# Optimization experiments

Measured on AMD Instinct MI355X. Metric: run time of the kernel, lower is better.

Reference implementation:

```python
import jax, jax.numpy as jnp
import numpy as np

D_MODEL = 512
N_HEADS = 8
D_K = D_MODEL // N_HEADS


def setup_inputs() -> dict:
    key = jax.random.key(0)
    ks = jax.random.split(key, 7)
    s = 1.0 / np.sqrt(D_MODEL)
    return {
        "x": jax.random.normal(ks[0], (2, 4096, D_MODEL), dtype=jnp.float32),
        "W_q": jax.random.normal(ks[1], (D_MODEL, D_MODEL), dtype=jnp.float32) * s,
        "W_k": jax.random.normal(ks[2], (D_MODEL, D_MODEL), dtype=jnp.float32) * s,
        "W_v": jax.random.normal(ks[3], (D_MODEL, D_MODEL), dtype=jnp.float32) * s,
        "b_v": jax.random.normal(ks[4], (D_MODEL,), dtype=jnp.float32) * s,
        "W_o": jax.random.normal(ks[5], (D_MODEL, D_MODEL), dtype=jnp.float32) * s,
        "b_o": jax.random.normal(ks[6], (D_MODEL,), dtype=jnp.float32) * s,
    }


def _split_heads(t):
    # [N, S, d_model] -> [N, H, S, d_k]
    N, S, _ = t.shape
    return t.reshape(N, S, N_HEADS, D_K).transpose(0, 2, 1, 3)


def reference(x, W_q, W_k, W_v, b_v, W_o, b_o):
    N, S, _ = x.shape
    # nn.Linear computes x @ W.T (+ b)
    Q = _split_heads(x @ W_q.T)
    K = _split_heads(x @ W_k.T)
    V = _split_heads(x @ W_v.T + b_v)
    scale = jnp.sqrt(jnp.asarray(D_K, x.dtype))
    scores = jnp.einsum('nhqd,nhkd->nhqk', Q, K) / scale  # [N,H,S,S]
    causal = jnp.tril(jnp.ones((S, S), dtype=bool))
    scores = jnp.where(causal, scores, -jnp.inf)
    attn = jax.nn.softmax(scores, axis=-1)
    out = jnp.einsum('nhqk,nhkd->nhqd', attn, V)  # [N,H,S,d_k]
    out = out.transpose(0, 2, 1, 3).reshape(N, S, D_MODEL)
    return out @ W_o.T + b_o
```

## Files before the change

### kernel.cpp

```cpp
#include <hip/hip_runtime.h>
#include <hip/hip_bf16.h>

#define NB 2
#define SEQ 4096
#define DM 512
#define NH 8
#define DKH 64
#define MTOT (NB*SEQ)

typedef __attribute__((ext_vector_type(4))) float f32x4;
typedef __attribute__((ext_vector_type(16))) float f32x16;
typedef __attribute__((ext_vector_type(8))) short bf16x8;
typedef __attribute__((ext_vector_type(2))) unsigned uint2v;

__device__ inline unsigned short f2bf(float f) {
    union { float f; unsigned int u; } v; v.f = f;
    unsigned int r = v.u + 0x7FFFu + ((v.u >> 16) & 1u);
    return (unsigned short)(r >> 16);
}

#define QSCALE 0.18033688011112042f

__global__ void cast_kernel(const float* __restrict__ x, const float* __restrict__ wq,
                            const float* __restrict__ wk, const float* __restrict__ wv,
                            const float* __restrict__ wo, unsigned short* __restrict__ dst) {
    const int NX = MTOT*DM;
    const int NW = DM*DM;
    int i4 = blockIdx.x * blockDim.x + threadIdx.x;
    long e = (long)i4 * 4;
    if (e >= NX + 4L*NW) return;
    const float* src; long off;
    if (e < NX)           { src = x;  off = e; }
    else if (e < NX+NW)   { src = wq; off = e - NX; }
    else if (e < NX+2*NW) { src = wk; off = e - NX - NW; }
    else if (e < NX+3*NW) { src = wv; off = e - NX - 2*NW; }
    else                  { src = wo; off = e - NX - 3*NW; }
    float4 v = *reinterpret_cast<const float4*>(src + off);
    ushort4 o;
    o.x = f2bf(v.x); o.y = f2bf(v.y); o.z = f2bf(v.z); o.w = f2bf(v.w);
    *reinterpret_cast<ushort4*>(dst + e) = o;
}

#define GEMM_KLOOP(APTR, BPTR, BROW, BCOL)                                         \
    f32x4 acc[4][4] = {};                                                          \
    for (int kt = 0; kt < 8; ++kt) {                                               \
        __syncthreads();                                                           \
        _Pragma("unroll")                                                          \
        for (int i = 0; i < 4; ++i) {                                              \
            int rbase = i*32 + wid*8;                                              \
            int row = rbase + (lane >> 3);                                         \
            int csrc = (lane & 7) ^ (row & 7);                                     \
            const unsigned short* asrc = Aptr_ + (long)((BROW)+row)*512 + kt*64 + csrc*8; \
            __builtin_amdgcn_global_load_lds(                                      \
                (const __attribute__((address_space(1))) unsigned int*)asrc,       \
                (__attribute__((address_space(3))) unsigned int*)&As[rbase*64], 16, 0, 0); \
            const unsigned short* bsrc = Bptr_ + (long)((BCOL)+row)*512 + kt*64 + csrc*8; \
            __builtin_amdgcn_global_load_lds(                                      \
                (const __attribute__((address_space(1))) unsigned int*)bsrc,       \
                (__attribute__((address_space(3))) unsigned int*)&Bs[rbase*64], 16, 0, 0); \
        }                                                                          \
        __syncthreads();                                                           \
        _Pragma("unroll")                                                          \
        for (int kk = 0; kk < 2; ++kk) {                                           \
            bf16x8 af[4], bfr[4];                                                  \
            _Pragma("unroll")                                                      \
            for (int mi = 0; mi < 4; ++mi) {                                       \
                int row = wr*64 + mi*16 + l15;                                     \
                int colb = (kk*32 + l4*8) * 2;                                     \
                af[mi] = *reinterpret_cast<const bf16x8*>(                         \
                    reinterpret_cast<const char*>(As) + row*128 + (colb ^ ((row&7)<<4))); \
            }                                                                      \
            _Pragma("unroll")                                                      \
            for (int ni = 0; ni < 4; ++ni) {                                       \
                int row = wc*64 + ni*16 + l15;                                     \
                int colb = (kk*32 + l4*8) * 2;                                     \
                bfr[ni] = *reinterpret_cast<const bf16x8*>(                        \
                    reinterpret_cast<const char*>(Bs) + row*128 + (colb ^ ((row&7)<<4))); \
            }                                                                      \
            _Pragma("unroll")                                                      \
            for (int mi = 0; mi < 4; ++mi)                                         \
                _Pragma("unroll")                                                  \
                for (int ni = 0; ni < 4; ++ni)                                     \
                    acc[mi][ni] = __builtin_amdgcn_mfma_f32_16x16x32_bf16(af[mi], bfr[ni], acc[mi][ni], 0, 0, 0); \
        }                                                                          \
    }

__global__ __launch_bounds__(256, 2) void gemm_qk(
    const unsigned short* __restrict__ A,
    const unsigned short* __restrict__ B,
    unsigned short* __restrict__ Qh, unsigned short* __restrict__ Kh)
{
    __shared__ __align__(16) unsigned short As[128*64];
    __shared__ __align__(16) unsigned short Bs[128*64];
    int tid = threadIdx.x;
    int wid = tid >> 6, lane = tid & 63;
    int wr = wid >> 1, wc = wid & 1;
    int brow = blockIdx.x * 128;
    int bcol = blockIdx.y * 128;
    int l15 = lane & 15, l4 = lane >> 4;
    const unsigned short* Aptr_ = A;
    const unsigned short* Bptr_ = B;

    GEMM_KLOOP(A, B, brow, bcol)

    #pragma unroll
    for (int mi = 0; mi < 4; ++mi) {
        #pragma unroll
        for (int ni = 0; ni < 4; ++ni) {
            #pragma unroll
            for (int r = 0; r < 4; ++r) {
                int row = brow + wr*64 + mi*16 + l4*4 + r;
                int col = bcol + wc*64 + ni*16 + l15;
                float v = acc[mi][ni][r];
                int which = col >> 9;
                int cw = col & 511;
                int h = cw >> 6, d = cw & 63;
                int b = row >> 12, s = row & 4095;
                int bh = b*NH + h;
                if (which == 0)
                    Qh[((long)(bh*SEQ + s))*DKH + d] = f2bf(v * QSCALE);
                else
                    Kh[((long)(bh*SEQ + s))*DKH + d] = f2bf(v);
            }
        }
    }
}

__global__ __launch_bounds__(256, 2) void gemm_v(
    const unsigned short* __restrict__ A,
    const unsigned short* __restrict__ B,
    const float* __restrict__ bv,
    unsigned short* __restrict__ Vt)
{
    __shared__ __align__(16) unsigned short As[128*64];
    __shared__ __align__(16) unsigned short Bs[128*64];
    __shared__ __align__(16) unsigned short Trs[128*136];
    int tid = threadIdx.x;
    int wid = tid >> 6, lane = tid & 63;
    int wr = wid >> 1, wc = wid & 1;
    int brow = blockIdx.x * 128;
    int bcol = 1024 + blockIdx.y * 128;
    int l15 = lane & 15, l4 = lane >> 4;
    const unsigned short* Aptr_ = A;
    const unsigned short* Bptr_ = B;

    GEMM_KLOOP(A, B, brow, bcol)

    #pragma unroll
    for (int mi = 0; mi < 4; ++mi) {
        #pragma unroll
        for (int ni = 0; ni < 4; ++ni) {
            #pragma unroll
            for (int r = 0; r < 4; ++r) {
                int rowLoc = wr*64 + mi*16 + l4*4 + r;
                int colLoc = wc*64 + ni*16 + l15;
                Trs[colLoc*136 + rowLoc] = f2bf(acc[mi][ni][r] + bv[(bcol + colLoc) & 511]);
            }
        }
    }
    __syncthreads();

    const int b = brow >> 12;
    const int stile = brow & 4095;
    const int hbase = (bcol - 1024) >> 6;
    #pragma unroll
    for (int pass = 0; pass < 8; ++pass) {
        int idx = pass*256 + tid;
        int dd = idx >> 4;
        int s8 = (idx & 15) << 3;
        bf16x8 vv = *reinterpret_cast<const bf16x8*>(&Trs[dd*136 + s8]);
        int bh = b*NH + hbase + (dd >> 6);
        int d = dd & 63;
        *reinterpret_cast<bf16x8*>(Vt + ((long)(bh*DKH + d))*SEQ + stile + s8) = vv;
    }
}

__global__ __launch_bounds__(256, 2) void gemm_out(
    const unsigned short* __restrict__ A,
    const unsigned short* __restrict__ B,
    const float* __restrict__ bias, float* __restrict__ Cout)
{
    __shared__ __align__(16) unsigned short As[128*64];
    __shared__ __align__(16) unsigned short Bs[128*64];
    int tid = threadIdx.x;
    int wid = tid >> 6, lane = tid & 63;
    int wr = wid >> 1, wc = wid & 1;
    int brow = blockIdx.x * 128;
    int bcol = blockIdx.y * 128;
    int l15 = lane & 15, l4 = lane >> 4;
    const unsigned short* Aptr_ = A;
    const unsigned short* Bptr_ = B;

    GEMM_KLOOP(A, B, brow, bcol)

    #pragma unroll
    for (int mi = 0; mi < 4; ++mi) {
        #pragma unroll
        for (int ni = 0; ni < 4; ++ni) {
            #pragma unroll
            for (int r = 0; r < 4; ++r) {
                int row = brow + wr*64 + mi*16 + l4*4 + r;
                int col = bcol + wc*64 + ni*16 + l15;
                Cout[(long)row*DM + col] = acc[mi][ni][r] + bias[col];
            }
        }
    }
}

#define PV_STEP_M(SV, VLS, KS, B0, OD0, OD1, LS)  do {                             \
        unsigned c0, c1, c2, c3;                                                   \
        float t0 = SV[B0+0], t1 = SV[B0+1], t2 = SV[B0+2], t3 = SV[B0+3];          \
        float t4 = SV[B0+4], t5 = SV[B0+5], t6 = SV[B0+6], t7 = SV[B0+7];          \
        asm("v_cvt_pk_bf16_f32 %0, %1, %2" : "=v"(c0) : "v"(t0), "v"(t1));         \
        asm("v_cvt_pk_bf16_f32 %0, %1, %2" : "=v"(c1) : "v"(t2), "v"(t3));         \
        asm("v_cvt_pk_bf16_f32 %0, %1, %2" : "=v"(c2) : "v"(t4), "v"(t5));         \
        asm("v_cvt_pk_bf16_f32 %0, %1, %2" : "=v"(c3) : "v"(t6), "v"(t7));         \
        uint2v sw0 = __builtin_amdgcn_permlane32_swap(c0, c2, false, false);       \
        uint2v sw1 = __builtin_amdgcn_permlane32_swap(c1, c3, false, false);       \
        union { unsigned u[4]; bf16x8 v; } pu;                                     \
        pu.u[0] = sw0[0]; pu.u[1] = sw1[0]; pu.u[2] = sw0[1]; pu.u[3] = sw1[1];    \
        bf16x8 vf0 = *reinterpret_cast<const bf16x8*>(VLS + l31*128      + (((KS)*32 + hi*16) ^ swz)); \
        OD0 = __builtin_amdgcn_mfma_f32_32x32x16_bf16(vf0, pu.v, OD0, 0, 0, 0);    \
        bf16x8 vf1 = *reinterpret_cast<const bf16x8*>(VLS + (32+l31)*128 + (((KS)*32 + hi*16) ^ swz)); \
        OD1 = __builtin_amdgcn_mfma_f32_32x32x16_bf16(vf1, pu.v, OD1, 0, 0, 0);    \
        LS  = __builtin_amdgcn_mfma_f32_32x32x16_bf16(onesv, pu.v, LS, 0, 0, 0);   \
    } while (0)

__global__ __launch_bounds__(256, 2) void attn_fm(
    const unsigned short* __restrict__ Qh,
    const unsigned short* __restrict__ Kh,
    const unsigned short* __restrict__ Vt,
    unsigned short* __restrict__ Obf)
{
    __shared__ __align__(16) unsigned short Klds[2][2][64*64];
    __shared__ __align__(16) unsigned short Vlds[2][2][64*64];
    const int tid = threadIdx.x;
    const int wid = tid >> 6, lane = tid & 63;
    const int g = wid & 1, p = wid >> 1;
    const int l31 = lane & 31;
    const int hi  = lane >> 5;
    const int bh  = blockIdx.x;
    const int j   = blockIdx.y;

    const unsigned short* Qbase = Qh + (long)bh*SEQ*DKH;
    const unsigned short* Kbase = Kh + (long)bh*SEQ*DKH;
    const unsigned short* Vbase = Vt + (long)bh*DKH*SEQ;
    const int swz = (l31 & 7) << 4;

    bf16x8 onesv;
    #pragma unroll
    for (int e = 0; e < 8; ++e) onesv[e] = (short)0x3F80;

    auto STAGE1 = [&](int pb, int b, int key0) {
        #pragma unroll
        for (int ii = 0; ii < 2; ++ii) {
            const int rbase = wid*16 + ii*8;
            const int row = rbase + (lane >> 3);
            const int ck = (lane & 7) ^ (row & 7);
            const unsigned short* ksrc = Kbase + (long)(key0 + row)*DKH + ck*8;
            __builtin_amdgcn_global_load_lds(
                (const __attribute__((address_space(1))) unsigned int*)ksrc,
                (__attribute__((address_space(3))) unsigned int*)&Klds[pb][b][rbase*64], 16, 0, 0);
            const unsigned short* vsrc = Vbase + (long)row*SEQ + key0 + ck*8;
            __builtin_amdgcn_global_load_lds(
                (const __attribute__((address_space(1))) unsigned int*)vsrc,
                (__attribute__((address_space(3))) unsigned int*)&Vlds[pb][b][rbase*64], 16, 0, 0);
        }
    };

    #pragma unroll 1
    for (int half = 0; half < 2; ++half) {
        const int tile = half ? (int)j : 63 - (int)j;
        const int q0w = tile*64 + g*32;
        const int q   = q0w + l31;
        const int nss = (tile >> 1) + 1;

        bf16x8 qf[4];
        #pragma unroll
        for (int kk = 0; kk < 4; ++kk)
            qf[kk] = *reinterpret_cast<const bf16x8*>(Qbase + (long)q*DKH + kk*16 + hi*8);

        f32x16 od0 = {}, od1 = {}, ls = {};

        STAGE1(0, 0, 0);
        if (tile >= 1) STAGE1(1, 0, 64);
        __syncthreads();

        #pragma unroll 1
        for (int ss = 0; ss < nss; ++ss) {
            const int nb = (ss + 1) & 1;
            if (2*(ss+1)     <= tile) STAGE1(0, nb, (2*(ss+1))     << 6);
            if (2*(ss+1) + 1 <= tile) STAGE1(1, nb, (2*(ss+1) + 1) << 6);

            const int kb = 2*ss + p;
            if (kb <= tile) {
                const int key0 = kb << 6;
                const char* kl = reinterpret_cast<const char*>(&Klds[p][ss & 1][0]);
                const char* vl = reinterpret_cast<const char*>(&Vlds[p][ss & 1][0]);

                bf16x8 kfr[4][2];
                #pragma unroll
                for (int kk = 0; kk < 4; ++kk) {
                    const int co = (kk*32 + hi*16) ^ swz;
                    kfr[kk][0] = *reinterpret_cast<const bf16x8*>(kl + l31*128      + co);
                    kfr[kk][1] = *reinterpret_cast<const bf16x8*>(kl + (32+l31)*128 + co);
                }
                f32x16 s0 = {}, s1 = {};
                __builtin_amdgcn_s_setprio(1);
                #pragma unroll
                for (int kk = 0; kk < 4; ++kk) {
                    s0 = __builtin_amdgcn_mfma_f32_32x32x16_bf16(kfr[kk][0], qf[kk], s0, 0, 0, 0);
                    s1 = __builtin_amdgcn_mfma_f32_32x32x16_bf16(kfr[kk][1], qf[kk], s1, 0, 0, 0);
                }
                __builtin_amdgcn_s_setprio(0);

                if (kb == tile) {
                    #pragma unroll
                    for (int r = 0; r < 16; ++r) {
                        const int ko = (r&3) + 8*(r>>2) + 4*hi;
                        if (key0 + ko > q)      s0[r] = -1e30f;
                        if (key0 + 32 + ko > q) s1[r] = -1e30f;
                    }
                }

                #pragma unroll
                for (int r = 0; r < 16; ++r) {
                    s0[r] = __builtin_amdgcn_exp2f(s0[r]);
                    s1[r] = __builtin_amdgcn_exp2f(s1[r]);
                }

                __builtin_amdgcn_s_setprio(1);
                PV_STEP_M(s0, vl, 0, 0, od0, od1, ls);
                PV_STEP_M(s0, vl, 1, 8, od0, od1, ls);
                PV_STEP_M(s1, vl, 2, 0, od0, od1, ls);
                PV_STEP_M(s1, vl, 3, 8, od0, od1, ls);
                __builtin_amdgcn_s_setprio(0);
            }
            __syncthreads();
        }

        float lsum = ls[0];
        char*  sod = reinterpret_cast<char*>(&Klds[g][0][0]);
        float* sml = reinterpret_cast<float*>(&Klds[g][1][0]);
        const int lswz = (lane & 7) << 4;
        if (p == 1) {
            #pragma unroll
            for (int i = 0; i < 4; ++i) {
                *reinterpret_cast<f32x4*>(sod + lane*128 + ((i*16) ^ lswz)) =
                    (f32x4){od0[i*4+0], od0[i*4+1], od0[i*4+2], od0[i*4+3]};
                *reinterpret_cast<f32x4*>(sod + lane*128 + (((i+4)*16) ^ lswz)) =
                    (f32x4){od1[i*4+0], od1[i*4+1], od1[i*4+2], od1[i*4+3]};
            }
            sml[lane] = lsum;
        }
        __syncthreads();
        if (p == 0) {
            lsum += sml[lane];
            #pragma unroll
            for (int i = 0; i < 4; ++i) {
                f32x4 t0 = *reinterpret_cast<const f32x4*>(sod + lane*128 + ((i*16) ^ lswz));
                f32x4 t1 = *reinterpret_cast<const f32x4*>(sod + lane*128 + (((i+4)*16) ^ lswz));
                #pragma unroll
                for (int k = 0; k < 4; ++k) {
                    od0[i*4+k] += t0[k];
                    od1[i*4+k] += t1[k];
                }
            }
            const float rls = 1.0f / lsum;
            const long obase = (long)((bh >> 3)*SEQ + q)*DM + (bh & 7)*DKH;
            #pragma unroll
            for (int rr = 0; rr < 4; ++rr) {
                ushort4 w0, w1;
                w0.x = f2bf(od0[rr*4+0]*rls); w0.y = f2bf(od0[rr*4+1]*rls);
                w0.z = f2bf(od0[rr*4+2]*rls); w0.w = f2bf(od0[rr*4+3]*rls);
                *reinterpret_cast<ushort4*>(Obf + obase + rr*8 + hi*4) = w0;
                w1.x = f2bf(od1[rr*4+0]*rls); w1.y = f2bf(od1[rr*4+1]*rls);
                w1.z = f2bf(od1[rr*4+2]*rls); w1.w = f2bf(od1[rr*4+3]*rls);
                *reinterpret_cast<ushort4*>(Obf + obase + 32 + rr*8 + hi*4) = w1;
            }
        }
        __syncthreads();
    }
}

extern "C" void kernel_launch(void* const* d_in, const int* in_sizes, int n_in,
                              void* d_out, int out_size, void* d_ws, size_t ws_size,
                              hipStream_t stream) {
    const float* x  = (const float*)d_in[0];
    const float* wq = (const float*)d_in[1];
    const float* wk = (const float*)d_in[2];
    const float* wv = (const float*)d_in[3];
    const float* bv = (const float*)d_in[4];
    const float* wo = (const float*)d_in[5];
    const float* bo = (const float*)d_in[6];
    float* out = (float*)d_out;

    unsigned short* ws = (unsigned short*)d_ws;
    unsigned short* Xbf  = ws;
    unsigned short* Wqkv = Xbf  + 4194304;
    unsigned short* Wob  = Wqkv + 786432;
    unsigned short* Qh   = Wob  + 262144;
    unsigned short* Kh   = Qh   + 4194304;
    unsigned short* Vt   = Kh   + 4194304;
    unsigned short* Obf  = Vt   + 4194304;

    cast_kernel<<<5120, 256, 0, stream>>>(x, wq, wk, wv, wo, Xbf);

    dim3 gqk(64, 8);
    gemm_qk<<<gqk, 256, 0, stream>>>(Xbf, Wqkv, Qh, Kh);
    dim3 gv(64, 4);
    gemm_v<<<gv, 256, 0, stream>>>(Xbf, Wqkv, bv, Vt);

    dim3 ga(16, 32);
    attn_fm<<<ga, 256, 0, stream>>>(Qh, Kh, Vt, Obf);

    dim3 go(64, 4);
    gemm_out<<<go, 256, 0, stream>>>(Obf, Wob, bo, out);
}
```

Baseline: 100.4 us.

## Split key halves across waves so each wave covers all 64 queries

Reassigns attention work so each wave processes both 32-query halves of the tile against its own 32-key half of a key block. K and V fragment LDS reads per wave drop, and the K fragments are reused across two query groups. The cost is more live accumulators and Q fragments, which raises register pressure. The final combine also becomes a 4-way LDS reduction done by a single wave.

```diff
diff --git a/kernel.cpp b/kernel.cpp
--- a/kernel.cpp
+++ b/kernel.cpp
@@ -207,7 +207,7 @@
     }
 }
 
-#define PV_STEP_M(SV, VLS, KS, B0, OD0, OD1, LS)  do {                             \
+#define REPACK(SV, B0, PU) do {                                                    \
         unsigned c0, c1, c2, c3;                                                   \
         float t0 = SV[B0+0], t1 = SV[B0+1], t2 = SV[B0+2], t3 = SV[B0+3];          \
         float t4 = SV[B0+4], t5 = SV[B0+5], t6 = SV[B0+6], t7 = SV[B0+7];          \
@@ -217,13 +217,21 @@
         asm("v_cvt_pk_bf16_f32 %0, %1, %2" : "=v"(c3) : "v"(t6), "v"(t7));         \
         uint2v sw0 = __builtin_amdgcn_permlane32_swap(c0, c2, false, false);       \
         uint2v sw1 = __builtin_amdgcn_permlane32_swap(c1, c3, false, false);       \
-        union { unsigned u[4]; bf16x8 v; } pu;                                     \
-        pu.u[0] = sw0[0]; pu.u[1] = sw1[0]; pu.u[2] = sw0[1]; pu.u[3] = sw1[1];    \
+        PU.u[0] = sw0[0]; PU.u[1] = sw1[0]; PU.u[2] = sw0[1]; PU.u[3] = sw1[1];    \
+    } while (0)
+
+#define PV2(SA, SB, VLS, KS, B0) do {                                              \
+        union { unsigned u[4]; bf16x8 v; } puA, puB;                               \
+        REPACK(SA, B0, puA);                                                       \
+        REPACK(SB, B0, puB);                                                       \
         bf16x8 vf0 = *reinterpret_cast<const bf16x8*>(VLS + l31*128      + (((KS)*32 + hi*16) ^ swz)); \
-        OD0 = __builtin_amdgcn_mfma_f32_32x32x16_bf16(vf0, pu.v, OD0, 0, 0, 0);    \
         bf16x8 vf1 = *reinterpret_cast<const bf16x8*>(VLS + (32+l31)*128 + (((KS)*32 + hi*16) ^ swz)); \
-        OD1 = __builtin_amdgcn_mfma_f32_32x32x16_bf16(vf1, pu.v, OD1, 0, 0, 0);    \
-        LS  = __builtin_amdgcn_mfma_f32_32x32x16_bf16(onesv, pu.v, LS, 0, 0, 0);   \
+        odA0 = __builtin_amdgcn_mfma_f32_32x32x16_bf16(vf0, puA.v, odA0, 0, 0, 0); \
+        odA1 = __builtin_amdgcn_mfma_f32_32x32x16_bf16(vf1, puA.v, odA1, 0, 0, 0); \
+        odB0 = __builtin_amdgcn_mfma_f32_32x32x16_bf16(vf0, puB.v, odB0, 0, 0, 0); \
+        odB1 = __builtin_amdgcn_mfma_f32_32x32x16_bf16(vf1, puB.v, odB1, 0, 0, 0); \
+        lsA  = __builtin_amdgcn_mfma_f32_32x32x16_bf16(onesv, puA.v, lsA, 0, 0, 0);\
+        lsB  = __builtin_amdgcn_mfma_f32_32x32x16_bf16(onesv, puB.v, lsB, 0, 0, 0);\
     } while (0)
 
 __global__ __launch_bounds__(256, 2) void attn_fm(
@@ -236,7 +244,7 @@
     __shared__ __align__(16) unsigned short Vlds[2][2][64*64];
     const int tid = threadIdx.x;
     const int wid = tid >> 6, lane = tid & 63;
-    const int g = wid & 1, p = wid >> 1;
+    const int p = wid & 1, h = wid >> 1;
     const int l31 = lane & 31;
     const int hi  = lane >> 5;
     const int bh  = blockIdx.x;
@@ -267,20 +275,27 @@
                 (__attribute__((address_space(3))) unsigned int*)&Vlds[pb][b][rbase*64], 16, 0, 0);
         }
     };
+    auto blk = [&](int b) -> char* {
+        return (b < 4) ? (reinterpret_cast<char*>(&Klds[0][0][0]) + b*8192)
+                       : (reinterpret_cast<char*>(&Vlds[0][0][0]) + (b-4)*8192);
+    };
+    float* smlBase = reinterpret_cast<float*>(reinterpret_cast<char*>(&Vlds[0][0][0]) + 16384);
 
     #pragma unroll 1
     for (int half = 0; half < 2; ++half) {
         const int tile = half ? (int)j : 63 - (int)j;
-        const int q0w = tile*64 + g*32;
-        const int q   = q0w + l31;
+        const int qA = tile*64 + l31;
+        const int qB = qA + 32;
         const int nss = (tile >> 1) + 1;
 
-        bf16x8 qf[4];
+        bf16x8 qfA[4], qfB[4];
         #pragma unroll
-        for (int kk = 0; kk < 4; ++kk)
-            qf[kk] = *reinterpret_cast<const bf16x8*>(Qbase + (long)q*DKH + kk*16 + hi*8);
-
-        f32x16 od0 = {}, od1 = {}, ls = {};
+        for (int kk = 0; kk < 4; ++kk) {
+            qfA[kk] = *reinterpret_cast<const bf16x8*>(Qbase + (long)qA*DKH + kk*16 + hi*8);
+            qfB[kk] = *reinterpret_cast<const bf16x8*>(Qbase + (long)qB*DKH + kk*16 + hi*8);
+        }
+
+        f32x16 odA0 = {}, odA1 = {}, odB0 = {}, odB1 = {}, lsA = {}, lsB = {};
 
         STAGE1(0, 0, 0);
         if (tile >= 1) STAGE1(1, 0, 64);
@@ -294,89 +309,107 @@
 
             const int kb = 2*ss + p;
             if (kb <= tile) {
-                const int key0 = kb << 6;
-                const char* kl = reinterpret_cast<const char*>(&Klds[p][ss & 1][0]);
+                const char* kl = reinterpret_cast<const char*>(&Klds[p][ss & 1][0]) + h*32*128;
                 const char* vl = reinterpret_cast<const char*>(&Vlds[p][ss & 1][0]);
-
-                bf16x8 kfr[4][2];
+                const int key0h = (kb << 6) + (h << 5);
+
+                bf16x8 kfr[4];
                 #pragma unroll
-                for (int kk = 0; kk < 4; ++kk) {
-                    const int co = (kk*32 + hi*16) ^ swz;
-                    kfr[kk][0] = *reinterpret_cast<const bf16x8*>(kl + l31*128      + co);
-                    kfr[kk][1] = *reinterpret_cast<const bf16x8*>(kl + (32+l31)*128 + co);
-                }
-                f32x16 s0 = {}, s1 = {};
+                for (int kk = 0; kk < 4; ++kk)
+                    kfr[kk] = *reinterpret_cast<const bf16x8*>(kl + l31*128 + ((kk*32 + hi*16) ^ swz));
+                f32x16 sA = {}, sB = {};
                 __builtin_amdgcn_s_setprio(1);
                 #pragma unroll
                 for (int kk = 0; kk < 4; ++kk) {
-                    s0 = __builtin_amdgcn_mfma_f32_32x32x16_bf16(kfr[kk][0], qf[kk], s0, 0, 0, 0);
-                    s1 = __builtin_amdgcn_mfma_f32_32x32x16_bf16(kfr[kk][1], qf[kk], s1, 0, 0, 0);
+                    sA = __builtin_amdgcn_mfma_f32_32x32x16_bf16(kfr[kk], qfA[kk], sA, 0, 0, 0);
+                    sB = __builtin_amdgcn_mfma_f32_32x32x16_bf16(kfr[kk], qfB[kk], sB, 0, 0, 0);
                 }
                 __builtin_amdgcn_s_setprio(0);
 
                 if (kb == tile) {
                     #pragma unroll
                     for (int r = 0; r < 16; ++r) {
-                        const int ko = (r&3) + 8*(r>>2) + 4*hi;
-                        if (key0 + ko > q)      s0[r] = -1e30f;
-                        if (key0 + 32 + ko > q) s1[r] = -1e30f;
+                        const int ko = key0h + (r&3) + 8*(r>>2) + 4*hi;
+                        if (ko > qA) sA[r] = -1e30f;
+                        if (ko > qB) sB[r] = -1e30f;
                     }
                 }
 
                 #pragma unroll
                 for (int r = 0; r < 16; ++r) {
-                    s0[r] = __builtin_amdgcn_exp2f(s0[r]);
-                    s1[r] = __builtin_amdgcn_exp2f(s1[r]);
+                    sA[r] = __builtin_amdgcn_exp2f(sA[r]);
+                    sB[r] = __builtin_amdgcn_exp2f(sB[r]);
                 }
 
                 __builtin_amdgcn_s_setprio(1);
-                PV_STEP_M(s0, vl, 0, 0, od0, od1, ls);
-                PV_STEP_M(s0, vl, 1, 8, od0, od1, ls);
-                PV_STEP_M(s1, vl, 2, 0, od0, od1, ls);
-                PV_STEP_M(s1, vl, 3, 8, od0, od1, ls);
+                PV2(sA, sB, vl, (2*h),     0);
+                PV2(sA, sB, vl, (2*h + 1), 8);
                 __builtin_amdgcn_s_setprio(0);
             }
             __syncthreads();
         }
 
-        float lsum = ls[0];
-        char*  sod = reinterpret_cast<char*>(&Klds[g][0][0]);
-        float* sml = reinterpret_cast<float*>(&Klds[g][1][0]);
+        float lA = lsA[0], lB = lsB[0];
         const int lswz = (lane & 7) << 4;
-        if (p == 1) {
+        if (wid != 0) {
+            char* dA = blk((wid-1)*2);
+            char* dB = blk((wid-1)*2 + 1);
             #pragma unroll
             for (int i = 0; i < 4; ++i) {
-                *reinterpret_cast<f32x4*>(sod + lane*128 + ((i*16) ^ lswz)) =
-                    (f32x4){od0[i*4+0], od0[i*4+1], od0[i*4+2], od0[i*4+3]};
-                *reinterpret_cast<f32x4*>(sod + lane*128 + (((i+4)*16) ^ lswz)) =
-                    (f32x4){od1[i*4+0], od1[i*4+1], od1[i*4+2], od1[i*4+3]};
-            }
-            sml[lane] = lsum;
+                *reinterpret_cast<f32x4*>(dA + lane*128 + ((i*16) ^ lswz)) =
+                    (f32x4){odA0[i*4+0], odA0[i*4+1], odA0[i*4+2], odA0[i*4+3]};
+                *reinterpret_cast<f32x4*>(dA + lane*128 + (((i+4)*16) ^ lswz)) =
+                    (f32x4){odA1[i*4+0], odA1[i*4+1], odA1[i*4+2], odA1[i*4+3]};
+                *reinterpret_cast<f32x4*>(dB + lane*128 + ((i*16) ^ lswz)) =
+                    (f32x4){odB0[i*4+0], odB0[i*4+1], odB0[i*4+2], odB0[i*4+3]};
+                *reinterpret_cast<f32x4*>(dB + lane*128 + (((i+4)*16) ^ lswz)) =
+                    (f32x4){odB1[i*4+0], odB1[i*4+1], odB1[i*4+2], odB1[i*4+3]};
+            }
+            smlBase[(wid-1)*128 + lane*2]     = lA;
+            smlBase[(wid-1)*128 + lane*2 + 1] = lB;
         }
         __syncthreads();
-        if (p == 0) {
-            lsum += sml[lane];
-            #pragma unroll
-            for (int i = 0; i < 4; ++i) {
-                f32x4 t0 = *reinterpret_cast<const f32x4*>(sod + lane*128 + ((i*16) ^ lswz));
-                f32x4 t1 = *reinterpret_cast<const f32x4*>(sod + lane*128 + (((i+4)*16) ^ lswz));
+        if (wid == 0) {
+            #pragma unroll 1
+            for (int w = 1; w <= 3; ++w) {
+                const char* dA = blk((w-1)*2);
+                const char* dB = blk((w-1)*2 + 1);
+                lA += smlBase[(w-1)*128 + lane*2];
+                lB += smlBase[(w-1)*128 + lane*2 + 1];
                 #pragma unroll
-                for (int k = 0; k < 4; ++k) {
-                    od0[i*4+k] += t0[k];
-                    od1[i*4+k] += t1[k];
+                for (int i = 0; i < 4; ++i) {
+                    f32x4 tA0 = *reinterpret_cast<const f32x4*>(dA + lane*128 + ((i*16) ^ lswz));
+                    f32x4 tA1 = *reinterpret_cast<const f32x4*>(dA + lane*128 + (((i+4)*16) ^ lswz));
+                    f32x4 tB0 = *reinterpret_cast<const f32x4*>(dB + lane*128 + ((i*16) ^ lswz));
+                    f32x4 tB1 = *reinterpret_cast<const f32x4*>(dB + lane*128 + (((i+4)*16) ^ lswz));
+                    #pragma unroll
+                    for (int k = 0; k < 4; ++k) {
+                        odA0[i*4+k] += tA0[k];
+                        odA1[i*4+k] += tA1[k];
+                        odB0[i*4+k] += tB0[k];
+                        odB1[i*4+k] += tB1[k];
+                    }
                 }
             }
-            const float rls = 1.0f / lsum;
-            const long obase = (long)((bh >> 3)*SEQ + q)*DM + (bh & 7)*DKH;
+            const float rlsA = 1.0f / lA;
+            const float rlsB = 1.0f / lB;
+            const long obaseA = (long)((bh >> 3)*SEQ + qA)*DM + (bh & 7)*DKH;
+            const long obaseB = (long)((bh >> 3)*SEQ + qB)*DM + (bh & 7)*DKH;
             #pragma unroll
             for (int rr = 0; rr < 4; ++rr) {
                 ushort4 w0, w1;
-                w0.x = f2bf(od0[rr*4+0]*rls); w0.y = f2bf(od0[rr*4+1]*rls);
-                w0.z = f2bf(od0[rr*4+2]*rls); w0.w = f2bf(od0[rr*4+3]*rls);
-                *reinterpret_cast<ushort4*>(Obf + obase + rr*8 + hi*4) = w0;
-                w1.x = f2bf(od1[rr*4+0]*rls); w1.y = f2bf(od1[rr*4+1]*rls);
-                w1.z = f2bf(od1[rr*4+2]*rls); w1.w = f2bf(od1[rr*4+3]*rls);
-                *reinterpret_cast<ushort4*>(Obf + obase + 32 + rr*8 + hi*4) = w1;
+                w0.x = f2bf(odA0[rr*4+0]*rlsA); w0.y = f2bf(odA0[rr*4+1]*rlsA);
+                w0.z = f2bf(odA0[rr*4+2]*rlsA); w0.w = f2bf(odA0[rr*4+3]*rlsA);
+                *reinterpret_cast<ushort4*>(Obf + obaseA + rr*8 + hi*4) = w0;
+                w1.x = f2bf(odA1[rr*4+0]*rlsA); w1.y = f2bf(odA1[rr*4+1]*rlsA);
+                w1.z = f2bf(odA1[rr*4+2]*rlsA); w1.w = f2bf(odA1[rr*4+3]*rlsA);
+                *reinterpret_cast<ushort4*>(Obf + obaseA + 32 + rr*8 + hi*4) = w1;
+                w0.x = f2bf(odB0[rr*4+0]*rlsB); w0.y = f2bf(odB0[rr*4+1]*rlsB);
+                w0.z = f2bf(odB0[rr*4+2]*rlsB); w0.w = f2bf(odB0[rr*4+3]*rlsB);
+                *reinterpret_cast<ushort4*>(Obf + obaseB + rr*8 + hi*4) = w0;
+                w1.x = f2bf(odB1[rr*4+0]*rlsB); w1.y = f2bf(odB1[rr*4+1]*rlsB);
+                w1.z = f2bf(odB1[rr*4+2]*rlsB); w1.w = f2bf(odB1[rr*4+3]*rlsB);
+                *reinterpret_cast<ushort4*>(Obf + obaseB + 32 + rr*8 + hi*4) = w1;
             }
         }
         __syncthreads();
```

Result: slower. 102.9 us (+2.5%).

## Restructure attention to one query tile per block with XCD-aware ordering

Applied to the files above, without the earlier changes.

Replaces the paired-tile load balancing (each block handled tiles 63-j and j) with one 64-query tile per block over a 1D grid of 1024 blocks. Blocks are ordered largest tile first and mapped so each head stays on one XCD. The two wave pairs now split each 64-key block into two 32-key halves rather than alternating whole key blocks. LDS is halved to allow 4 blocks per CU. This targets better occupancy and L2 locality, but it depends on the scheduler to balance uneven causal work, and the 32-key split gives each wave less work per barrier.

```diff
diff --git a/kernel.cpp b/kernel.cpp
--- a/kernel.cpp
+++ b/kernel.cpp
@@ -226,32 +226,45 @@
         LS  = __builtin_amdgcn_mfma_f32_32x32x16_bf16(onesv, pu.v, LS, 0, 0, 0);   \
     } while (0)
 
-__global__ __launch_bounds__(256, 2) void attn_fm(
+__global__ __launch_bounds__(256, 4) void attn_fm(
     const unsigned short* __restrict__ Qh,
     const unsigned short* __restrict__ Kh,
     const unsigned short* __restrict__ Vt,
     unsigned short* __restrict__ Obf)
 {
-    __shared__ __align__(16) unsigned short Klds[2][2][64*64];
-    __shared__ __align__(16) unsigned short Vlds[2][2][64*64];
+    __shared__ __align__(16) unsigned short Kc[2][64*64];
+    __shared__ __align__(16) unsigned short Vc[2][64*64];
     const int tid = threadIdx.x;
     const int wid = tid >> 6, lane = tid & 63;
     const int g = wid & 1, p = wid >> 1;
     const int l31 = lane & 31;
     const int hi  = lane >> 5;
-    const int bh  = blockIdx.x;
-    const int j   = blockIdx.y;
+
+    const int id   = blockIdx.x;
+    const int xcd  = id & 7;
+    const int rest = id >> 3;
+    const int bh   = xcd + ((rest & 1) << 3);
+    const int t    = 63 - (rest >> 1);
 
     const unsigned short* Qbase = Qh + (long)bh*SEQ*DKH;
     const unsigned short* Kbase = Kh + (long)bh*SEQ*DKH;
     const unsigned short* Vbase = Vt + (long)bh*DKH*SEQ;
+
+    const int q0w = t*64 + g*32;
+    const int q   = q0w + l31;
+    const int nu  = t + 1;
     const int swz = (l31 & 7) << 4;
 
+    bf16x8 qf[4];
+    #pragma unroll
+    for (int kk = 0; kk < 4; ++kk)
+        qf[kk] = *reinterpret_cast<const bf16x8*>(Qbase + (long)q*DKH + kk*16 + hi*8);
+
     bf16x8 onesv;
     #pragma unroll
     for (int e = 0; e < 8; ++e) onesv[e] = (short)0x3F80;
 
-    auto STAGE1 = [&](int pb, int b, int key0) {
+    auto STAGE = [&](int b, int key0) {
         #pragma unroll
         for (int ii = 0; ii < 2; ++ii) {
             const int rbase = wid*16 + ii*8;
@@ -260,126 +273,98 @@
             const unsigned short* ksrc = Kbase + (long)(key0 + row)*DKH + ck*8;
             __builtin_amdgcn_global_load_lds(
                 (const __attribute__((address_space(1))) unsigned int*)ksrc,
-                (__attribute__((address_space(3))) unsigned int*)&Klds[pb][b][rbase*64], 16, 0, 0);
+                (__attribute__((address_space(3))) unsigned int*)&Kc[b][rbase*64], 16, 0, 0);
             const unsigned short* vsrc = Vbase + (long)row*SEQ + key0 + ck*8;
             __builtin_amdgcn_global_load_lds(
                 (const __attribute__((address_space(1))) unsigned int*)vsrc,
-                (__attribute__((address_space(3))) unsigned int*)&Vlds[pb][b][rbase*64], 16, 0, 0);
+                (__attribute__((address_space(3))) unsigned int*)&Vc[b][rbase*64], 16, 0, 0);
         }
     };
 
+    f32x16 od0 = {}, od1 = {}, ls = {};
+
+    STAGE(0, 0);
+    __syncthreads();
+    int cur = 0;
+
     #pragma unroll 1
-    for (int half = 0; half < 2; ++half) {
-        const int tile = half ? (int)j : 63 - (int)j;
-        const int q0w = tile*64 + g*32;
-        const int q   = q0w + l31;
-        const int nss = (tile >> 1) + 1;
-
-        bf16x8 qf[4];
+    for (int u = 0; u < nu; ++u) {
+        if (u + 1 < nu) STAGE(cur ^ 1, (u + 1) << 6);
+        const char* kl = reinterpret_cast<const char*>(&Kc[cur][0]) + p*32*128;
+        const char* vl = reinterpret_cast<const char*>(&Vc[cur][0]);
+
+        bf16x8 kfr[4];
         #pragma unroll
         for (int kk = 0; kk < 4; ++kk)
-            qf[kk] = *reinterpret_cast<const bf16x8*>(Qbase + (long)q*DKH + kk*16 + hi*8);
-
-        f32x16 od0 = {}, od1 = {}, ls = {};
-
-        STAGE1(0, 0, 0);
-        if (tile >= 1) STAGE1(1, 0, 64);
+            kfr[kk] = *reinterpret_cast<const bf16x8*>(kl + l31*128 + ((kk*32 + hi*16) ^ swz));
+        f32x16 sv = {};
+        __builtin_amdgcn_s_setprio(1);
+        #pragma unroll
+        for (int kk = 0; kk < 4; ++kk)
+            sv = __builtin_amdgcn_mfma_f32_32x32x16_bf16(kfr[kk], qf[kk], sv, 0, 0, 0);
+        __builtin_amdgcn_s_setprio(0);
+
+        if (u == t) {
+            const int kbase = (u << 6) + (p << 5);
+            #pragma unroll
+            for (int r = 0; r < 16; ++r) {
+                const int ko = (r&3) + 8*(r>>2) + 4*hi;
+                if (kbase + ko > q) sv[r] = -1e30f;
+            }
+        }
+
+        #pragma unroll
+        for (int r = 0; r < 16; ++r)
+            sv[r] = __builtin_amdgcn_exp2f(sv[r]);
+
+        __builtin_amdgcn_s_setprio(1);
+        PV_STEP_M(sv, vl, (2*p),     0, od0, od1, ls);
+        PV_STEP_M(sv, vl, (2*p + 1), 8, od0, od1, ls);
+        __builtin_amdgcn_s_setprio(0);
+
         __syncthreads();
-
-        #pragma unroll 1
-        for (int ss = 0; ss < nss; ++ss) {
-            const int nb = (ss + 1) & 1;
-            if (2*(ss+1)     <= tile) STAGE1(0, nb, (2*(ss+1))     << 6);
-            if (2*(ss+1) + 1 <= tile) STAGE1(1, nb, (2*(ss+1) + 1) << 6);
-
-            const int kb = 2*ss + p;
-            if (kb <= tile) {
-                const int key0 = kb << 6;
-                const char* kl = reinterpret_cast<const char*>(&Klds[p][ss & 1][0]);
-                const char* vl = reinterpret_cast<const char*>(&Vlds[p][ss & 1][0]);
-
-                bf16x8 kfr[4][2];
-                #pragma unroll
-                for (int kk = 0; kk < 4; ++kk) {
-                    const int co = (kk*32 + hi*16) ^ swz;
-                    kfr[kk][0] = *reinterpret_cast<const bf16x8*>(kl + l31*128      + co);
-                    kfr[kk][1] = *reinterpret_cast<const bf16x8*>(kl + (32+l31)*128 + co);
-                }
-                f32x16 s0 = {}, s1 = {};
-                __builtin_amdgcn_s_setprio(1);
-                #pragma unroll
-                for (int kk = 0; kk < 4; ++kk) {
-                    s0 = __builtin_amdgcn_mfma_f32_32x32x16_bf16(kfr[kk][0], qf[kk], s0, 0, 0, 0);
-                    s1 = __builtin_amdgcn_mfma_f32_32x32x16_bf16(kfr[kk][1], qf[kk], s1, 0, 0, 0);
-                }
-                __builtin_amdgcn_s_setprio(0);
-
-                if (kb == tile) {
-                    #pragma unroll
-                    for (int r = 0; r < 16; ++r) {
-                        const int ko = (r&3) + 8*(r>>2) + 4*hi;
-                        if (key0 + ko > q)      s0[r] = -1e30f;
-                        if (key0 + 32 + ko > q) s1[r] = -1e30f;
-                    }
-                }
-
-                #pragma unroll
-                for (int r = 0; r < 16; ++r) {
-                    s0[r] = __builtin_amdgcn_exp2f(s0[r]);
-                    s1[r] = __builtin_amdgcn_exp2f(s1[r]);
-                }
-
-                __builtin_amdgcn_s_setprio(1);
-                PV_STEP_M(s0, vl, 0, 0, od0, od1, ls);
-                PV_STEP_M(s0, vl, 1, 8, od0, od1, ls);
-                PV_STEP_M(s1, vl, 2, 0, od0, od1, ls);
-                PV_STEP_M(s1, vl, 3, 8, od0, od1, ls);
-                __builtin_amdgcn_s_setprio(0);
+        cur ^= 1;
+    }
+
+    float lsum = ls[0];
+    char*  sod = reinterpret_cast<char*>(&Kc[g][0]);
+    float* sml = reinterpret_cast<float*>(&Vc[g][0]);
+    const int lswz = (lane & 7) << 4;
+    if (p == 1) {
+        #pragma unroll
+        for (int i = 0; i < 4; ++i) {
+            *reinterpret_cast<f32x4*>(sod + lane*128 + ((i*16) ^ lswz)) =
+                (f32x4){od0[i*4+0], od0[i*4+1], od0[i*4+2], od0[i*4+3]};
+            *reinterpret_cast<f32x4*>(sod + lane*128 + (((i+4)*16) ^ lswz)) =
+                (f32x4){od1[i*4+0], od1[i*4+1], od1[i*4+2], od1[i*4+3]};
+        }
+        sml[lane] = lsum;
+    }
+    __syncthreads();
+    if (p == 0) {
+        lsum += sml[lane];
+        #pragma unroll
+        for (int i = 0; i < 4; ++i) {
+            f32x4 t0 = *reinterpret_cast<const f32x4*>(sod + lane*128 + ((i*16) ^ lswz));
+            f32x4 t1 = *reinterpret_cast<const f32x4*>(sod + lane*128 + (((i+4)*16) ^ lswz));
+            #pragma unroll
+            for (int k = 0; k < 4; ++k) {
+                od0[i*4+k] += t0[k];
+                od1[i*4+k] += t1[k];
             }
-            __syncthreads();
-        }
-
-        float lsum = ls[0];
-        char*  sod = reinterpret_cast<char*>(&Klds[g][0][0]);
-        float* sml = reinterpret_cast<float*>(&Klds[g][1][0]);
-        const int lswz = (lane & 7) << 4;
-        if (p == 1) {
-            #pragma unroll
-            for (int i = 0; i < 4; ++i) {
-                *reinterpret_cast<f32x4*>(sod + lane*128 + ((i*16) ^ lswz)) =
-                    (f32x4){od0[i*4+0], od0[i*4+1], od0[i*4+2], od0[i*4+3]};
-                *reinterpret_cast<f32x4*>(sod + lane*128 + (((i+4)*16) ^ lswz)) =
-                    (f32x4){od1[i*4+0], od1[i*4+1], od1[i*4+2], od1[i*4+3]};
-            }
-            sml[lane] = lsum;
-        }
-        __syncthreads();
-        if (p == 0) {
-            lsum += sml[lane];
-            #pragma unroll
-            for (int i = 0; i < 4; ++i) {
-                f32x4 t0 = *reinterpret_cast<const f32x4*>(sod + lane*128 + ((i*16) ^ lswz));
-                f32x4 t1 = *reinterpret_cast<const f32x4*>(sod + lane*128 + (((i+4)*16) ^ lswz));
-                #pragma unroll
-                for (int k = 0; k < 4; ++k) {
-                    od0[i*4+k] += t0[k];
-                    od1[i*4+k] += t1[k];
-                }
-            }
-            const float rls = 1.0f / lsum;
-            const long obase = (long)((bh >> 3)*SEQ + q)*DM + (bh & 7)*DKH;
-            #pragma unroll
-            for (int rr = 0; rr < 4; ++rr) {
-                ushort4 w0, w1;
-                w0.x = f2bf(od0[rr*4+0]*rls); w0.y = f2bf(od0[rr*4+1]*rls);
-                w0.z = f2bf(od0[rr*4+2]*rls); w0.w = f2bf(od0[rr*4+3]*rls);
-                *reinterpret_cast<ushort4*>(Obf + obase + rr*8 + hi*4) = w0;
-                w1.x = f2bf(od1[rr*4+0]*rls); w1.y = f2bf(od1[rr*4+1]*rls);
-                w1.z = f2bf(od1[rr*4+2]*rls); w1.w = f2bf(od1[rr*4+3]*rls);
-                *reinterpret_cast<ushort4*>(Obf + obase + 32 + rr*8 + hi*4) = w1;
-            }
-        }
-        __syncthreads();
+        }
+        const float rls = 1.0f / lsum;
+        const long obase = (long)((bh >> 3)*SEQ + q)*DM + (bh & 7)*DKH;
+        #pragma unroll
+        for (int rr = 0; rr < 4; ++rr) {
+            ushort4 w0, w1;
+            w0.x = f2bf(od0[rr*4+0]*rls); w0.y = f2bf(od0[rr*4+1]*rls);
+            w0.z = f2bf(od0[rr*4+2]*rls); w0.w = f2bf(od0[rr*4+3]*rls);
+            *reinterpret_cast<ushort4*>(Obf + obase + rr*8 + hi*4) = w0;
+            w1.x = f2bf(od1[rr*4+0]*rls); w1.y = f2bf(od1[rr*4+1]*rls);
+            w1.z = f2bf(od1[rr*4+2]*rls); w1.w = f2bf(od1[rr*4+3]*rls);
+            *reinterpret_cast<ushort4*>(Obf + obase + 32 + rr*8 + hi*4) = w1;
+        }
     }
 }
 
@@ -411,7 +396,7 @@
     dim3 gv(64, 4);
     gemm_v<<<gv, 256, 0, stream>>>(Xbf, Wqkv, bv, Vt);
 
-    dim3 ga(16, 32);
+    dim3 ga(1024);
     attn_fm<<<ga, 256, 0, stream>>>(Qh, Kh, Vt, Obf);
 
     dim3 go(64, 4);
```

Measured after the change: 104.1 us. 1.04x slower.
